# Kernel optimization log

Hardware: AMD Instinct MI355X
Metric: run time of the kernel (lower is better)

The kernel has to match this reference:

```python
import jax, jax.numpy as jnp
import numpy as np

R = 12            # search_radius
P = 2 * R + 1     # 25x25 search window
DIV = 512.0       # self.div_num; T = DIV**-0.5


def _relu_l2norm(x, axis=1, eps=1e-12):
    # matches F.relu followed by F.normalize(p=2, dim=1)
    x = jax.nn.relu(x)
    n = jnp.sqrt(jnp.sum(x * x, axis=axis, keepdims=True))
    return x / jnp.maximum(n, eps)


def setup_inputs() -> dict:
    key = jax.random.key(0)
    k1, k2 = jax.random.split(key)
    feat1_video = jax.random.normal(k1, (8, 512, 4, 30, 30), dtype=jnp.float32)  # r50_feat1 (pre relu/norm)
    feat2_img = jax.random.normal(k2, (8, 512, 30, 30), dtype=jnp.float32)       # img_feat2 (pre relu/norm)
    return {"feat1_video": feat1_video, "feat2_img": feat2_img}


def reference(feat1_video, feat2_img):
    # relu + channel L2-normalize, as in forward() before compute_corr_softmax
    video = _relu_l2norm(feat1_video)          # [B,C,T,H,W]  -> r50_feat2 arg
    patch = _relu_l2norm(feat2_img)            # [B,C,H,W]    -> patch_feat1 arg
    B, C, T, H, W = video.shape

    vpad = jnp.pad(video, ((0, 0), (0, 0), (0, 0), (R, R), (R, R)))

    # all 625 (dh, dw) window offsets, vmapped into one fused correlation
    offsets = jnp.stack(
        jnp.meshgrid(jnp.arange(P), jnp.arange(P), indexing="ij"), axis=-1
    ).reshape(-1, 2)  # [P*P, 2]

    def shift_corr(off):
        win = jax.lax.dynamic_slice(
            vpad, (0, 0, 0, off[0], off[1]), (B, C, T, H, W)
        )
        return jnp.einsum("bcthw,bchw->bthw", win, patch)

    corr = jax.vmap(shift_corr)(offsets)               # [P*P, B, T, H, W]
    corr = jnp.transpose(corr, (1, 2, 0, 3, 4))        # [B, T, P*P, H, W]

    # torch: div by div_num**-0.5, then softmax(corr / T) with T = div_num**-0.5
    Tparam = DIV ** (-0.5)
    corr = corr / (DIV ** (-0.5)) / Tparam             # == corr * 512
    sm = jax.nn.softmax(corr, axis=2)

    # validity mask: output pixel y with shift h=dh-R is valid iff 0 <= y+h < H
    dh = jnp.arange(P)
    ys = jnp.arange(H)
    xs = jnp.arange(W)
    valid_h = ((ys[None, :] + dh[:, None] - R) >= 0) & ((ys[None, :] + dh[:, None] - R) < H)  # [P,H]
    valid_w = ((xs[None, :] + dh[:, None] - R) >= 0) & ((xs[None, :] + dh[:, None] - R) < W)  # [P,W]
    valid = valid_h[:, None, :, None] & valid_w[None, :, None, :]  # [P,P,H,W]
    valid = valid.reshape(P * P, H, W)

    out = jnp.where(valid[None, None], sm, jnp.float32(-1.0))      # [B,T,P*P,H,W]
    return out.reshape(B, T, P, P, H, W)
```

## Files before the change

### kernel.cpp

```cpp
#include <hip/hip_runtime.h>

#define RR 12
#define PD 25
#define PP 625
#define HH 30
#define WW 30
#define HWD 900
#define CD 512
#define BD 8
#define TD 4
#define CSTRIDE 628
#define ROWPKB 32768
#define QSCALE 16129.0f
#define EXPK (512.0f / QSCALE)

typedef __attribute__((ext_vector_type(4))) int i32x4;
typedef __attribute__((ext_vector_type(16))) int i32x16;

__global__ __launch_bounds__(256) void norm_pack_kernel(const float* __restrict__ inP,
                                                        const float* __restrict__ inV,
                                                        unsigned char* __restrict__ outA,
                                                        unsigned char* __restrict__ outB) {
    int row = blockIdx.x;
    int plane = blockIdx.y;
    const float* in;
    size_t base;
    int c_stride;
    unsigned char* ob;
    if (plane < 8) {
        in = inP; c_stride = HWD;
        base = (size_t)plane * CD * HWD + row * WW;
        ob = outA + (size_t)(plane * 30 + row) * ROWPKB;
    } else {
        int bt = plane - 8;
        int b = bt >> 2, t = bt & 3;
        in = inV; c_stride = TD * HWD;
        base = (size_t)b * CD * (TD * HWD) + (size_t)t * HWD + row * WW;
        ob = outB + (size_t)(bt * 30 + row) * ROWPKB;
    }
    __shared__ float tile[30][516];
    __shared__ float inv[30];
    int tid = threadIdx.x;
    for (int it = 0; it < 64; ++it) {
        int lin = it * 256 + tid;
        int c = lin >> 5, p = lin & 31;
        if (p < 30) tile[p][c] = fmaxf(in[base + (size_t)c * c_stride + p], 0.f);
    }
    __syncthreads();
    if ((tid >> 3) < 30) {
        int p = tid >> 3, s8 = tid & 7;
        float acc = 0.f;
#pragma unroll
        for (int j = 0; j < 16; ++j) {
            const float4 v = *reinterpret_cast<const float4*>(&tile[p][(s8 + j * 8) * 4]);
            acc += v.x * v.x + v.y * v.y + v.z * v.z + v.w * v.w;
        }
        acc += __shfl_xor(acc, 1);
        acc += __shfl_xor(acc, 2);
        acc += __shfl_xor(acc, 4);
        if (s8 == 0) inv[p] = 1.0f / fmaxf(sqrtf(acc), 1e-12f);
    }
    __syncthreads();
    for (int sl = tid; sl < 1024; sl += 256) {
        int ks = sl >> 6, ln = sl & 63;
        int x = ln & 31;
        if (x > 29) x = 29;
        int kb = ks * 32 + (ln >> 5) * 16;
        float iv = inv[x];
        union { signed char c[16]; i32x4 v; } p1, p2;
#pragma unroll
        for (int j = 0; j < 16; ++j) {
            float nv = tile[x][kb + j] * iv;
            float s1 = rintf(nv * 127.f);
            float r = nv * 127.f - s1;
            float s2 = rintf(r * 254.f);
            p1.c[j] = (signed char)(int)s1;
            p2.c[j] = (signed char)(int)s2;
        }
        *(i32x4*)(ob + (size_t)ks * 2048 + ln * 16) = p1.v;
        *(i32x4*)(ob + (size_t)ks * 2048 + 1024 + ln * 16) = p2.v;
    }
}

__global__ __launch_bounds__(1024, 4) void corr_kernel(
    const unsigned char* __restrict__ Apk, const unsigned char* __restrict__ Bpk,
    float* __restrict__ out) {
    int gid = blockIdx.x;
    int r = gid & 7;
    int x_ = gid >> 3;
    int btl = x_ / 30;
    int h = x_ - btl * 30;
    int bt = r * 4 + btl;
    int b = r;

    __shared__ __attribute__((aligned(16))) float corr[HH * CSTRIDE];
    __shared__ unsigned char alds[ROWPKB];
    __shared__ float is_lds[HH];
    int tid = threadIdx.x;
    int wid = tid >> 6, lane = tid & 63;

    {
        float4 z = {0.f, 0.f, 0.f, 0.f};
        float4* cz = (float4*)corr;
        for (int i = tid; i < (HH * CSTRIDE) / 4; i += 1024) cz[i] = z;
    }
    {
        const uint4* src = (const uint4*)(Apk + (size_t)(b * 30 + h) * ROWPKB);
        uint4* dst = (uint4*)alds;
#pragma unroll
        for (int i = 0; i < 2; ++i) dst[i * 1024 + tid] = src[i * 1024 + tid];
    }
    const unsigned char* bplane = Bpk + (size_t)bt * 30 * ROWPKB + lane * 16;
    int dh_lo = max(0, RR - h);
    int dh_hi = min(PD - 1, HH - 1 + RR - h);
    __syncthreads();

    const unsigned char* albase = alds + lane * 16;
    for (int dh = dh_lo + wid; dh <= dh_hi; dh += 16) {
        int y = h + dh - RR;
        const unsigned char* bbase = bplane + (size_t)y * ROWPKB;
        i32x16 s11, s12, s21, s22;
#pragma unroll
        for (int i = 0; i < 16; ++i) { s11[i] = 0; s12[i] = 0; s21[i] = 0; s22[i] = 0; }
#pragma unroll 8
        for (int ks = 0; ks < 16; ++ks) {
            i32x4 a1 = *(const i32x4*)(albase + ks * 2048);
            i32x4 a2 = *(const i32x4*)(albase + ks * 2048 + 1024);
            i32x4 b1 = *(const i32x4*)(bbase + ks * 2048);
            i32x4 b2 = *(const i32x4*)(bbase + ks * 2048 + 1024);
            s11 = __builtin_amdgcn_mfma_i32_32x32x32_i8(a1, b1, s11, 0, 0, 0);
            s12 = __builtin_amdgcn_mfma_i32_32x32x32_i8(a1, b2, s12, 0, 0, 0);
            s21 = __builtin_amdgcn_mfma_i32_32x32x32_i8(a2, b1, s21, 0, 0, 0);
            s22 = __builtin_amdgcn_mfma_i32_32x32x32_i8(a2, b2, s22, 0, 0, 0);
        }
        int x = lane & 31;
        if (x < 30) {
            int rbase = 4 * (lane >> 5);
#pragma unroll
            for (int rr = 0; rr < 16; ++rr) {
                int w = (rr & 3) + 8 * (rr >> 2) + rbase;
                int dw = x - w + RR;
                if (w < 30 && (unsigned)dw < (unsigned)PD) {
                    float c = fmaf((float)(s12[rr] + s21[rr]), 1.0f / 254.0f,
                                   (float)s11[rr]) +
                              (float)s22[rr] * (1.0f / 64516.0f);
                    corr[w * CSTRIDE + dh * PD + dw] = c;
                }
            }
        }
    }
    __syncthreads();

    for (int w = wid; w < WW; w += 16) {
        float m = 0.f;
        for (int i = lane; i < PP; i += 64) m = fmaxf(m, corr[w * CSTRIDE + i]);
        m = fmaxf(m, __shfl_xor(m, 1));
        m = fmaxf(m, __shfl_xor(m, 2));
        m = fmaxf(m, __shfl_xor(m, 4));
        m = fmaxf(m, __shfl_xor(m, 8));
        m = fmaxf(m, __shfl_xor(m, 16));
        m = fmaxf(m, __shfl_xor(m, 32));
        float s = 0.f;
        for (int i = lane; i < PP; i += 64) {
            float e = __expf(EXPK * (corr[w * CSTRIDE + i] - m));
            s += e;
            corr[w * CSTRIDE + i] = e;
        }
        s += __shfl_xor(s, 1);
        s += __shfl_xor(s, 2);
        s += __shfl_xor(s, 4);
        s += __shfl_xor(s, 8);
        s += __shfl_xor(s, 16);
        s += __shfl_xor(s, 32);
        if (lane == 0) is_lds[w] = 1.0f / s;
    }
    __syncthreads();

    float* obase = out + (size_t)bt * PP * HWD + h * WW;
    for (int idx = tid; idx < PP * 32; idx += 1024) {
        int w = idx & 31;
        if (w < 30) {
            int i = idx >> 5;
            int dh = i / 25, dw = i - dh * 25;
            bool valid = ((unsigned)(h + dh - RR) < (unsigned)HH) &&
                         ((unsigned)(w + dw - RR) < (unsigned)WW);
            float val = -1.0f;
            if (valid) val = corr[w * CSTRIDE + i] * is_lds[w];
            __builtin_nontemporal_store(val, &obase[(size_t)i * HWD + w]);
        }
    }
}

extern "C" void kernel_launch(void* const* d_in, const int* in_sizes, int n_in,
                              void* d_out, int out_size, void* d_ws, size_t ws_size,
                              hipStream_t stream) {
    const float* feat1 = (const float*)d_in[0];
    const float* feat2 = (const float*)d_in[1];
    float* out = (float*)d_out;
    unsigned char* Apk = (unsigned char*)d_ws;
    unsigned char* Bpk = Apk + (size_t)BD * 30 * ROWPKB;

    norm_pack_kernel<<<dim3(30, 40), 256, 0, stream>>>(feat2, feat1, Apk, Bpk);
    corr_kernel<<<dim3(960), 1024, 0, stream>>>(Apk, Bpk, out);
}
```

Before: 118.5 us.

## Split int8 MFMA work across wave pairs and vectorize norm loads

The correlation loop now assigns each dh row to a pair of waves: one handles the high-part A slice, the other the low-part slice, each issuing two MFMAs per k-step instead of one wave issuing four. Partial results are combined into shared memory with atomicAdd, which doubles wave-level parallelism across the up to 25 dh rows. The cost is LDS atomics and the float summation order. Separately, the normalization kernel loads input pairs as float2 to halve load instructions.

```diff
diff --git a/kernel.cpp b/kernel.cpp
--- a/kernel.cpp
+++ b/kernel.cpp
@@ -41,10 +41,15 @@
     __shared__ float tile[30][516];
     __shared__ float inv[30];
     int tid = threadIdx.x;
-    for (int it = 0; it < 64; ++it) {
+    for (int it = 0; it < 32; ++it) {
         int lin = it * 256 + tid;
-        int c = lin >> 5, p = lin & 31;
-        if (p < 30) tile[p][c] = fmaxf(in[base + (size_t)c * c_stride + p], 0.f);
+        int c = lin >> 4, pg = lin & 15;
+        if (pg < 15) {
+            const float2 v = *reinterpret_cast<const float2*>(
+                &in[base + (size_t)c * c_stride + pg * 2]);
+            tile[pg * 2][c] = fmaxf(v.x, 0.f);
+            tile[pg * 2 + 1][c] = fmaxf(v.y, 0.f);
+        }
     }
     __syncthreads();
     if ((tid >> 3) < 30) {
@@ -98,6 +103,8 @@
     __shared__ float is_lds[HH];
     int tid = threadIdx.x;
     int wid = tid >> 6, lane = tid & 63;
+    int wa = wid & 1;
+    int pr = wid >> 1;
 
     {
         float4 z = {0.f, 0.f, 0.f, 0.f};
@@ -115,36 +122,33 @@
     int dh_hi = min(PD - 1, HH - 1 + RR - h);
     __syncthreads();
 
-    const unsigned char* albase = alds + lane * 16;
-    for (int dh = dh_lo + wid; dh <= dh_hi; dh += 16) {
+    const unsigned char* albase = alds + lane * 16 + wa * 1024;
+    float wscale = wa ? (1.0f / 254.0f) : 1.0f;
+    int x = lane & 31;
+    int rbase = 4 * (lane >> 5);
+
+    for (int dh = dh_lo + pr; dh <= dh_hi; dh += 8) {
         int y = h + dh - RR;
         const unsigned char* bbase = bplane + (size_t)y * ROWPKB;
-        i32x16 s11, s12, s21, s22;
-#pragma unroll
-        for (int i = 0; i < 16; ++i) { s11[i] = 0; s12[i] = 0; s21[i] = 0; s22[i] = 0; }
+        i32x16 sA, sB;
+#pragma unroll
+        for (int i = 0; i < 16; ++i) { sA[i] = 0; sB[i] = 0; }
 #pragma unroll 8
         for (int ks = 0; ks < 16; ++ks) {
-            i32x4 a1 = *(const i32x4*)(albase + ks * 2048);
-            i32x4 a2 = *(const i32x4*)(albase + ks * 2048 + 1024);
+            i32x4 a = *(const i32x4*)(albase + ks * 2048);
             i32x4 b1 = *(const i32x4*)(bbase + ks * 2048);
             i32x4 b2 = *(const i32x4*)(bbase + ks * 2048 + 1024);
-            s11 = __builtin_amdgcn_mfma_i32_32x32x32_i8(a1, b1, s11, 0, 0, 0);
-            s12 = __builtin_amdgcn_mfma_i32_32x32x32_i8(a1, b2, s12, 0, 0, 0);
-            s21 = __builtin_amdgcn_mfma_i32_32x32x32_i8(a2, b1, s21, 0, 0, 0);
-            s22 = __builtin_amdgcn_mfma_i32_32x32x32_i8(a2, b2, s22, 0, 0, 0);
-        }
-        int x = lane & 31;
+            sA = __builtin_amdgcn_mfma_i32_32x32x32_i8(a, b1, sA, 0, 0, 0);
+            sB = __builtin_amdgcn_mfma_i32_32x32x32_i8(a, b2, sB, 0, 0, 0);
+        }
         if (x < 30) {
-            int rbase = 4 * (lane >> 5);
 #pragma unroll
             for (int rr = 0; rr < 16; ++rr) {
                 int w = (rr & 3) + 8 * (rr >> 2) + rbase;
                 int dw = x - w + RR;
                 if (w < 30 && (unsigned)dw < (unsigned)PD) {
-                    float c = fmaf((float)(s12[rr] + s21[rr]), 1.0f / 254.0f,
-                                   (float)s11[rr]) +
-                              (float)s22[rr] * (1.0f / 64516.0f);
-                    corr[w * CSTRIDE + dh * PD + dw] = c;
+                    float val = fmaf((float)sB[rr], 1.0f / 254.0f, (float)sA[rr]) * wscale;
+                    atomicAdd(&corr[w * CSTRIDE + dh * PD + dw], val);
                 }
             }
         }
```

Result: slower. 211.1 us (+78.1%).
